# Optimization experiments

Hardware: AMD Instinct MI355X
Metric: run time of the kernel (lower is better)

## Reference

```python
import jax, jax.numpy as jnp
import numpy as np
from jax import lax

# config constants (match init_kwargs)
SEQ_LEN = 512
PRED_LEN = 96
ENC_IN = 64
D_MODEL = 128
E_LAYERS = 2
GRAPH_SCALE = 16
GRAPH_RANK = 8
TCN_KERNEL = 3
TCN_DILATION = 2
BATCH = 16


def setup_inputs() -> dict:
    key = jax.random.key(0)
    ks = jax.random.split(key, 12)
    s = 0.02
    inp = {
        "x_enc": jax.random.normal(ks[0], (BATCH, SEQ_LEN, ENC_IN), jnp.float32),
        "x_mark_enc": jnp.zeros((BATCH, SEQ_LEN, 4), jnp.float32),
        "x_dec": jnp.zeros((BATCH, PRED_LEN, ENC_IN), jnp.float32),
        "x_mark_dec": jnp.zeros((BATCH, PRED_LEN, 4), jnp.float32),
        # value embedding (scalar -> d_model)
        "w_emb": jax.random.normal(ks[1], (1, D_MODEL), jnp.float32) * s,
        "b_emb": jnp.zeros((D_MODEL,), jnp.float32),
        # stacked dilated causal conv layers [L, K, Cin, Cout]
        "conv_w": jax.random.normal(ks[2], (E_LAYERS, TCN_KERNEL, D_MODEL, D_MODEL), jnp.float32) * s,
        "conv_b": jnp.zeros((E_LAYERS, D_MODEL), jnp.float32),
        # low-rank graph generator projections
        "gg_w1": jax.random.normal(ks[3], (D_MODEL, GRAPH_RANK), jnp.float32) * s,
        "gg_b1": jnp.zeros((GRAPH_RANK,), jnp.float32),
        "gg_w2": jax.random.normal(ks[4], (D_MODEL, GRAPH_RANK), jnp.float32) * s,
        "gg_b2": jnp.zeros((GRAPH_RANK,), jnp.float32),
        # head: Linear(d_model * num_tokens, pred_len)
        "head_w": jax.random.normal(ks[5], (D_MODEL * SEQ_LEN, PRED_LEN), jnp.float32) * s,
        "head_b": jnp.zeros((PRED_LEN,), jnp.float32),
    }
    return inp


def _tcn(x_enc, w_emb, b_emb, conv_w, conv_b):
    # x_enc: [B, L, N] -> channel-independent per-variable encoding -> [B, N, L, D]
    B, L, N = x_enc.shape
    h = x_enc.transpose(0, 2, 1).reshape(B * N, L, 1) @ w_emb + b_emb  # [B*N, L, D]
    for i in range(conv_w.shape[0]):
        dil = TCN_DILATION ** i
        pad = (TCN_KERNEL - 1) * dil
        hp = jnp.pad(h, ((0, 0), (pad, 0), (0, 0)))  # causal left pad
        y = lax.conv_general_dilated(
            hp, conv_w[i], window_strides=(1,), padding="VALID",
            rhs_dilation=(dil,), dimension_numbers=("NWC", "WIO", "NWC"),
        ) + conv_b[i]
        h = jax.nn.gelu(y) + h  # residual
    return h.reshape(B, N, L, -1)


def _forward(x_enc, w_emb, b_emb, conv_w, conv_b, gg_w1, gg_b1, gg_w2, gg_b2, head_w, head_b):
    h_time = _tcn(x_enc, w_emb, b_emb, conv_w, conv_b)  # [B, N, L, D]
    B, N, L, D = h_time.shape
    S = L // GRAPH_SCALE  # number of segments (L divisible by scale)
    h_seg = h_time.reshape(B, N, S, GRAPH_SCALE, D)
    z = h_seg.mean(axis=3)  # [B, N, S, D] segment summaries
    # low-rank graph generation for all segments at once
    e1 = z @ gg_w1 + gg_b1  # [B, N, S, r]
    e2 = z @ gg_w2 + gg_b2
    scores = jnp.einsum("bnsr,bmsr->bsnm", e1, e2) / jnp.asarray(np.sqrt(GRAPH_RANK), z.dtype)
    adj = jax.nn.softmax(scores, axis=-1)  # [B, S, N, N] row-stochastic
    # adjacency temporal-smoothness regularizer: sum_s mean|adj_s - adj_{s-1}|
    reg = jnp.sum(jnp.mean(jnp.abs(adj[:, 1:] - adj[:, :-1]), axis=(0, 2, 3)))
    # graph-weighted feature mixing per segment
    h_mix = jnp.einsum("bsnm,bmscd->bnscd", adj, h_seg).reshape(B, N, L, D)
    # head over flattened (token, dim)
    out = h_mix.reshape(B, N, L * D) @ head_w + head_b  # [B, N, pred_len]
    return out.transpose(0, 2, 1), reg  # [B, pred_len, N]


def reference(x_enc, x_mark_enc, x_dec, x_mark_dec, w_emb, b_emb, conv_w, conv_b,
              gg_w1, gg_b1, gg_w2, gg_b2, head_w, head_b):
    # x_mark_enc / x_dec / x_mark_dec are unused by forecast path (faithful to source)
    return _forward(x_enc, w_emb, b_emb, conv_w, conv_b, gg_w1, gg_b1, gg_w2, gg_b2, head_w, head_b)
```

## Files before the change

### kernel.cpp

```cpp
#include <hip/hip_runtime.h>
#include <hip/hip_bf16.h>


#define BATCH 16
#define SEQ 512
#define NVAR 64
#define DM 128
#define SEG 32
#define SCL 16
#define RNK 8
#define PRED 96
#define BN (BATCH * NVAR)
#define ROWLEN (SEQ * DM)

typedef unsigned short ushort_t;
typedef __attribute__((ext_vector_type(8))) short short8;
typedef __attribute__((ext_vector_type(4))) float f32x4;

__device__ inline float bf2f(ushort_t u) {
    union { unsigned int i; float f; } x;
    x.i = ((unsigned int)u) << 16;
    return x.f;
}
__device__ inline ushort_t f2bf(float f) {
    union { float f; unsigned int i; } u;
    u.f = f;
    unsigned int x = u.i;
    return (ushort_t)((x + 0x7fffu + ((x >> 16) & 1u)) >> 16);
}
__device__ inline unsigned int pkbf(float a, float b) {
    __hip_bfloat162 h = __float22bfloat162_rn(make_float2(a, b));
    union { __hip_bfloat162 h2; unsigned int u; } c;
    c.h2 = h;
    return c.u;
}
__device__ inline float blo(unsigned int u) {
    union { unsigned int i; float f; } x;
    x.i = u << 16;
    return x.f;
}
__device__ inline float bhi(unsigned int u) {
    union { unsigned int i; float f; } x;
    x.i = u & 0xFFFF0000u;
    return x.f;
}
__device__ inline float gelu_fast(float x) {
    float x2 = x * x;
    float t2 = x * fmaf(-0.10294854f, x2, -2.3022584f);
    float e;
    asm("v_exp_f32 %0, %1" : "=v"(e) : "v"(t2));
    return x * __builtin_amdgcn_rcpf(1.0f + e);
}

__global__ __launch_bounds__(256) void prep(
    const float* __restrict__ conv_w, const float* __restrict__ w_emb,
    const float* __restrict__ b_emb, const float* __restrict__ conv_b,
    const float* __restrict__ head_w, const float* __restrict__ head_b,
    ushort_t* __restrict__ WTf, float* __restrict__ Acoef,
    float* __restrict__ Bias3, ushort_t* __restrict__ HWf,
    float* __restrict__ out, float* __restrict__ regacc) {
    __shared__ float ts[32 * 97];
    int bid = blockIdx.x;
    if (bid == 0 && threadIdx.x == 0) regacc[0] = 0.f;
    if (bid < 512) {
        int bx = bid >> 7, ci = bid & 127;
        if (threadIdx.x < 128) {
            int co = threadIdx.x;
            if (bx < 3) {
                int kt = ci >> 5, quad = (ci >> 3) & 3, j = ci & 7;
                int ng = co >> 4, col = co & 15;
                int lane = quad * 16 + col;
                WTf[((((size_t)bx * 4 + kt) * 8 + ng) * 64 + lane) * 8 + j] =
                    f2bf(conv_w[(size_t)(3 + bx) * 16384 + (size_t)ci * 128 + co]);
            } else if (ci == 0) {
                float a0 = 0.f, a1 = 0.f, a2 = 0.f, c0 = 0.f, c1 = 0.f, c2 = 0.f;
                for (int k = 0; k < 128; ++k) {
                    float we = w_emb[k], be = b_emb[k];
                    float w0 = conv_w[((size_t)(0 * 128 + k)) * 128 + co];
                    float w1 = conv_w[((size_t)(1 * 128 + k)) * 128 + co];
                    float w2 = conv_w[((size_t)(2 * 128 + k)) * 128 + co];
                    a0 += we * w0; c0 += be * w0;
                    a1 += we * w1; c1 += be * w1;
                    a2 += we * w2; c2 += be * w2;
                }
                Acoef[0 * 128 + co] = a0;
                Acoef[1 * 128 + co] = a1;
                Acoef[2 * 128 + co] = a2;
                float b0 = conv_b[co];
                Bias3[0 * 128 + co] = b0 + c2;
                Bias3[1 * 128 + co] = b0 + c1 + c2;
                Bias3[2 * 128 + co] = b0 + c0 + c1 + c2;
            }
        }
    } else if (bid < 1536) {
        int k32p = bid - 512;
        int s = k32p >> 5, t = k32p & 31;
        int kbase = (s * 64 + t) * 32;
        const float* src = head_w + (size_t)kbase * 96;
        for (int idx = threadIdx.x; idx < 3072; idx += 256) {
            int kk = idx / 96, p = idx - kk * 96;
            ts[kk * 97 + p] = src[idx];
        }
        __syncthreads();
        unsigned int* ob32 =
            reinterpret_cast<unsigned int*>(HWf + (size_t)k32p * 3072);
        for (int odx = threadIdx.x; odx < 1536; odx += 256) {
            int p = odx >> 4, kk = (odx & 15) * 2;
            ob32[odx] = pkbf(ts[kk * 97 + p], ts[(kk + 1) * 97 + p]);
        }
    } else {
        int idx = (bid - 1536) * 256 + threadIdx.x;
        if (idx < BATCH * PRED * NVAR) {
            int p = (idx >> 6) % PRED;
            out[idx] = head_b[p];
        }
    }
}

__global__ __launch_bounds__(256) void hw_prep(
    const float* __restrict__ head_w, ushort_t* __restrict__ HWf, int kh) {
    __shared__ float ts[32 * 97];
    int k32p = blockIdx.x;
    int s = k32p >> 5, t = k32p & 31;
    int kbase = (s * 64 + kh * 32 + t) * 32;
    const float* src = head_w + (size_t)kbase * 96;
    for (int idx = threadIdx.x; idx < 3072; idx += 256) {
        int kk = idx / 96, p = idx - kk * 96;
        ts[kk * 97 + p] = src[idx];
    }
    __syncthreads();
    unsigned int* ob32 =
        reinterpret_cast<unsigned int*>(HWf + (size_t)k32p * 3072);
    for (int odx = threadIdx.x; odx < 1536; odx += 256) {
        int p = odx >> 4, kk = (odx & 15) * 2;
        ob32[odx] = pkbf(ts[kk * 97 + p], ts[(kk + 1) * 97 + p]);
    }
}

__global__ __launch_bounds__(256, 4) void tcn_mfma(
    const float* __restrict__ x, const float* __restrict__ w_emb,
    const float* __restrict__ b_emb, const float* __restrict__ Acoef,
    const float* __restrict__ Bias3, const ushort_t* __restrict__ WTf,
    const float* __restrict__ conv_b,
    const float* __restrict__ gw1, const float* __restrict__ gb1,
    const float* __restrict__ gw2, const float* __restrict__ gb2,
    ushort_t* __restrict__ h2, float* __restrict__ e1, float* __restrict__ e2) {
    __shared__ __align__(16) ushort_t h1s[68 * 136];
    __shared__ float xs[70];
    __shared__ float zbuf[4 * 136];

    int bn = blockIdx.x;
    int b = bn >> 6, n = bn & 63;
    int chunk = blockIdx.y;
    int l0 = chunk * 64;
    int tid = threadIdx.x;

    {
        const float* xb = x + (size_t)b * SEQ * NVAR + n;
        if (tid < 70) {
            int l = l0 - 6 + tid;
            xs[tid] = (l >= 0) ? xb[(size_t)l * NVAR] : 0.0f;
        }
    }
    __syncthreads();

    {
        int dp = (tid & 63) * 2;
        float2 A0 = *reinterpret_cast<const float2*>(&Acoef[0 * 128 + dp]);
        float2 A1 = *reinterpret_cast<const float2*>(&Acoef[1 * 128 + dp]);
        float2 A2 = *reinterpret_cast<const float2*>(&Acoef[2 * 128 + dp]);
        float2 BF = *reinterpret_cast<const float2*>(&Bias3[2 * 128 + dp]);
        float2 we2 = *reinterpret_cast<const float2*>(&w_emb[dp]);
        float2 be2 = *reinterpret_cast<const float2*>(&b_emb[dp]);
#pragma unroll
        for (int i = 0; i < 17; ++i) {
            int row = (tid >> 6) + 4 * i;
            int l = l0 - 4 + row;
            unsigned int pk = 0;
            if (l >= 0) {
                float x0 = xs[row], x1 = xs[row + 1], x2 = xs[row + 2];
                float2 bias = BF;
                if (l < 2)
                    bias = *reinterpret_cast<const float2*>(&Bias3[l * 128 + dp]);
                float y0 = fmaf(x0, A0.x, fmaf(x1, A1.x, fmaf(x2, A2.x, bias.x)));
                float y1 = fmaf(x0, A0.y, fmaf(x1, A1.y, fmaf(x2, A2.y, bias.y)));
                float r0 = gelu_fast(y0) + fmaf(x2, we2.x, be2.x);
                float r1 = gelu_fast(y1) + fmaf(x2, we2.y, be2.y);
                pk = pkbf(r0, r1);
            }
            *reinterpret_cast<unsigned int*>(&h1s[row * 136 + dp]) = pk;
        }
    }
    __syncthreads();

    int lane = tid & 63;
    int wv = tid >> 6;
    int quad = lane >> 4;
    int col = lane & 15;
    int cobase = wv * 32;

    f32x4 acc2[4][2];
#pragma unroll
    for (int mt = 0; mt < 4; ++mt)
#pragma unroll
        for (int nt = 0; nt < 2; ++nt)
            acc2[mt][nt] = (f32x4){0.f, 0.f, 0.f, 0.f};

#pragma unroll
    for (int tap = 0; tap < 3; ++tap) {
        short8 wf0[4], wf1[4];
#pragma unroll
        for (int kt = 0; kt < 4; ++kt) {
            const ushort_t* bp =
                WTf + ((((size_t)tap * 4 + kt) * 8 + wv * 2) * 64 + lane) * 8;
            wf0[kt] = *(const short8*)bp;
            wf1[kt] = *(const short8*)(bp + 512);
        }
#pragma unroll
        for (int kt = 0; kt < 4; ++kt) {
            int kc = kt * 32 + quad * 8;
#pragma unroll
            for (int mt = 0; mt < 4; ++mt) {
                short8 hf = *(const short8*)&h1s[(mt * 16 + col + 2 * tap) * 136 + kc];
                acc2[mt][0] = __builtin_amdgcn_mfma_f32_16x16x32_bf16(wf0[kt], hf, acc2[mt][0], 0, 0, 0);
                acc2[mt][1] = __builtin_amdgcn_mfma_f32_16x16x32_bf16(wf1[kt], hf, acc2[mt][1], 0, 0, 0);
            }
        }
    }

    {
        uint2 res[4][2];
#pragma unroll
        for (int mt = 0; mt < 4; ++mt) {
            int li = mt * 16 + col;
#pragma unroll
            for (int nt = 0; nt < 2; ++nt) {
                int co = cobase + nt * 16 + quad * 4;
                res[mt][nt] = *reinterpret_cast<const uint2*>(
                    &h1s[(li + 4) * 136 + co]);
            }
        }
        __syncthreads();
        float4 bias[2];
        bias[0] = *reinterpret_cast<const float4*>(&conv_b[DM + cobase + quad * 4]);
        bias[1] = *reinterpret_cast<const float4*>(&conv_b[DM + cobase + 16 + quad * 4]);
#pragma unroll
        for (int mt = 0; mt < 4; ++mt) {
            int li = mt * 16 + col;
#pragma unroll
            for (int nt = 0; nt < 2; ++nt) {
                int co = cobase + nt * 16 + quad * 4;
                float h0 = gelu_fast(acc2[mt][nt][0] + bias[nt].x) + blo(res[mt][nt].x);
                float h1 = gelu_fast(acc2[mt][nt][1] + bias[nt].y) + bhi(res[mt][nt].x);
                float h2v = gelu_fast(acc2[mt][nt][2] + bias[nt].z) + blo(res[mt][nt].y);
                float h3 = gelu_fast(acc2[mt][nt][3] + bias[nt].w) + bhi(res[mt][nt].y);
                uint2 pk;
                pk.x = pkbf(h0, h1);
                pk.y = pkbf(h2v, h3);
                *reinterpret_cast<uint2*>(&h1s[li * 136 + co]) = pk;
            }
        }
    }
    __syncthreads();

    {
        ushort_t* orow = h2 + (size_t)bn * ROWLEN + (size_t)l0 * 128;
#pragma unroll
        for (int i = 0; i < 4; ++i) {
            int q = tid + 256 * i;
            int row = q >> 4, c8 = (q & 15) * 8;
            *(short8*)&orow[row * 128 + c8] = *(const short8*)&h1s[row * 136 + c8];
        }
    }
    {
        int sl = tid >> 6;
        int dp = (tid & 63) * 2;
        float a0 = 0.0f, a1 = 0.0f;
#pragma unroll
        for (int c = 0; c < SCL; ++c) {
            unsigned int u = *reinterpret_cast<const unsigned int*>(
                &h1s[(sl * 16 + c) * 136 + dp]);
            a0 += blo(u);
            a1 += bhi(u);
        }
        zbuf[sl * 136 + dp] = a0 * 0.0625f;
        zbuf[sl * 136 + dp + 1] = a1 * 0.0625f;
    }
    __syncthreads();
    {
        int outi = tid >> 2;
        int part = tid & 3;
        int sl = outi >> 4;
        int which = (outi >> 3) & 1;
        int r = outi & 7;
        const float* w = which ? gw2 : gw1;
        float a = 0.0f;
#pragma unroll 8
        for (int i = 0; i < 32; ++i) {
            int d = i * 4 + part;
            a += zbuf[sl * 136 + d] * w[d * RNK + r];
        }
        a += __shfl_xor(a, 1, 64);
        a += __shfl_xor(a, 2, 64);
        if (part == 0) {
            a += (which ? gb2 : gb1)[r];
            int s = chunk * 4 + sl;
            (which ? e2 : e1)[(((size_t)b * SEG + s) * NVAR + n) * RNK + r] = a;
        }
    }
}

__global__ __launch_bounds__(256) void g_gemm(
    const ushort_t* __restrict__ h2, const ushort_t* __restrict__ HWf,
    float* __restrict__ G, int kh, int first) {
    __shared__ __align__(16) ushort_t As[2][64 * 72];
    int s = blockIdx.x;
    int bnt = blockIdx.y;
    int bn0 = bnt * 64;
    int kbase = kh * 1024;
    int lane = threadIdx.x & 63, wv = threadIdx.x >> 6;
    int quad = lane >> 4, col = lane & 15;
    int mh = wv & 1;
    int ph = wv >> 1;
    int p0 = ph * 48 + col;

    int arow = threadIdx.x >> 2, akq = (threadIdx.x & 3) * 16;
    const ushort_t* aptr =
        h2 + (size_t)(bn0 + arow) * ROWLEN + (size_t)s * 2048 + kbase + akq;
    const ushort_t* hb =
        HWf + (size_t)s * 98304 + (size_t)p0 * 32 + quad * 8;

    f32x4 acc[3][2];
#pragma unroll
    for (int i = 0; i < 3; ++i)
#pragma unroll
        for (int j = 0; j < 2; ++j) acc[i][j] = (f32x4){0.f, 0.f, 0.f, 0.f};

    short8 pa0 = *(const short8*)aptr;
    short8 pa1 = *(const short8*)(aptr + 8);
    short8 pf[2][2][3];
#pragma unroll
    for (int kk = 0; kk < 2; ++kk)
#pragma unroll
        for (int i = 0; i < 3; ++i)
            pf[0][kk][i] = *(const short8*)(hb + kk * 3072 + i * 512);
    *(short8*)&As[0][arow * 72 + akq] = pa0;
    *(short8*)&As[0][arow * 72 + akq + 8] = pa1;
    __syncthreads();

#pragma unroll
    for (int kt = 0; kt < 16; ++kt) {
        const int par = kt & 1;
        if (kt < 15) {
            const ushort_t* ap = aptr + (kt + 1) * 64;
            pa0 = *(const short8*)ap;
            pa1 = *(const short8*)(ap + 8);
            const ushort_t* fb = hb + (size_t)(kt + 1) * 6144;
#pragma unroll
            for (int kk = 0; kk < 2; ++kk)
#pragma unroll
                for (int i = 0; i < 3; ++i)
                    pf[par ^ 1][kk][i] =
                        *(const short8*)(fb + kk * 3072 + i * 512);
        }
#pragma unroll
        for (int kk = 0; kk < 2; ++kk) {
            int kc = kk * 32 + quad * 8;
#pragma unroll
            for (int j = 0; j < 2; ++j) {
                short8 bnfr =
                    *(const short8*)&As[par][(mh * 32 + j * 16 + col) * 72 + kc];
#pragma unroll
                for (int i = 0; i < 3; ++i)
                    acc[i][j] = __builtin_amdgcn_mfma_f32_16x16x32_bf16(
                        pf[par][kk][i], bnfr, acc[i][j], 0, 0, 0);
            }
        }
        if (kt < 15) {
            *(short8*)&As[par ^ 1][arow * 72 + akq] = pa0;
            *(short8*)&As[par ^ 1][arow * 72 + akq + 8] = pa1;
        }
        __syncthreads();
    }

#pragma unroll
    for (int i = 0; i < 3; ++i)
#pragma unroll
        for (int j = 0; j < 2; ++j)
#pragma unroll
            for (int r = 0; r < 4; ++r) {
                int p = ph * 48 + i * 16 + quad * 4 + r;
                int m = mh * 32 + j * 16 + col;
                size_t o = (((size_t)s * BATCH + bnt) * PRED + p) * NVAR + m;
                if (first) G[o] = acc[i][j][r];
                else G[o] += acc[i][j][r];
            }
}

__global__ __launch_bounds__(256) void out_mix(
    const float* __restrict__ e1, const float* __restrict__ e2,
    const float* __restrict__ G, float* __restrict__ out,
    float* __restrict__ regacc) {
    __shared__ float adjn[2][32][65];
    __shared__ float Gs[96][65];
    __shared__ float e2s[3][64][8];
    __shared__ float e1s[3][32][8];
    __shared__ float wsum[4];
    int b = blockIdx.x, sg = blockIdx.y, nh = blockIdx.z;
    int s0 = sg * 2;
    int wv = threadIdx.x >> 6, lane = threadIdx.x & 63;

    for (int idx = threadIdx.x; idx < 3 * 64 * 8; idx += 256) {
        int j = idx >> 9, m = (idx >> 3) & 63, r = idx & 7;
        int s = s0 - 1 + j;
        e2s[j][m][r] = (s >= 0)
            ? e2[(((size_t)b * SEG + s) * NVAR + m) * RNK + r] : 0.0f;
    }
    for (int idx = threadIdx.x; idx < 3 * 32 * 8; idx += 256) {
        int j = idx >> 8, nl = (idx >> 3) & 31, r = idx & 7;
        int s = s0 - 1 + j;
        e1s[j][nl][r] = (s >= 0)
            ? e1[(((size_t)b * SEG + s) * NVAR + nh * 32 + nl) * RNK + r] : 0.0f;
    }
    __syncthreads();

    float regsum = 0.0f;
    for (int t = 0; t < 8; ++t) {
        int nl = wv * 8 + t;
        float a[3];
#pragma unroll
        for (int j = 0; j < 3; ++j) {
            float sc = 0.0f;
#pragma unroll
            for (int r = 0; r < 8; ++r) sc += e1s[j][nl][r] * e2s[j][lane][r];
            sc *= 0.35355339059327373f;
            float mx = sc;
            for (int off = 32; off; off >>= 1)
                mx = fmaxf(mx, __shfl_xor(mx, off, 64));
            float ex = __expf(sc - mx);
            float sm = ex;
            for (int off = 32; off; off >>= 1) sm += __shfl_xor(sm, off, 64);
            a[j] = ex * __builtin_amdgcn_rcpf(sm);
        }
        if (s0 > 0) regsum += fabsf(a[1] - a[0]);
        regsum += fabsf(a[2] - a[1]);
        adjn[0][nl][lane] = a[1];
        adjn[1][nl][lane] = a[2];
    }
    __syncthreads();

    int pg = threadIdx.x >> 4;
    int ng = threadIdx.x & 15;
    float acc[6][2];
#pragma unroll
    for (int j = 0; j < 6; ++j) { acc[j][0] = 0.f; acc[j][1] = 0.f; }

#pragma unroll
    for (int ss = 0; ss < 2; ++ss) {
        int s = s0 + ss;
#pragma unroll
        for (int i = 0; i < 6; ++i) {
            int q = threadIdx.x + 256 * i;
            int row = q >> 4, mq = (q & 15) * 4;
            float4 v = *reinterpret_cast<const float4*>(
                &G[(((size_t)s * BATCH + b) * PRED + row) * NVAR + mq]);
            Gs[row][mq + 0] = v.x; Gs[row][mq + 1] = v.y;
            Gs[row][mq + 2] = v.z; Gs[row][mq + 3] = v.w;
        }
        __syncthreads();
#pragma unroll 4
        for (int m = 0; m < 64; ++m) {
            float a0 = adjn[ss][ng * 2 + 0][m];
            float a1 = adjn[ss][ng * 2 + 1][m];
#pragma unroll
            for (int j = 0; j < 6; ++j) {
                float g = Gs[pg * 6 + j][m];
                acc[j][0] += g * a0;
                acc[j][1] += g * a1;
            }
        }
        __syncthreads();
    }
#pragma unroll
    for (int j = 0; j < 6; ++j)
#pragma unroll
        for (int i = 0; i < 2; ++i) {
            int p = pg * 6 + j, n = nh * 32 + ng * 2 + i;
            atomicAdd(&out[((size_t)b * PRED + p) * NVAR + n], acc[j][i]);
        }
    for (int off = 32; off; off >>= 1) regsum += __shfl_xor(regsum, off, 64);
    if (lane == 0) wsum[wv] = regsum;
    __syncthreads();
    if (threadIdx.x == 0)
        atomicAdd(regacc, wsum[0] + wsum[1] + wsum[2] + wsum[3]);
}

__global__ void fin(const float* __restrict__ regacc, float* __restrict__ out,
                    int out_size) {
    out[out_size - 1] = regacc[0] * (1.0f / 65536.0f);
}

extern "C" void kernel_launch(void* const* d_in, const int* in_sizes, int n_in,
                              void* d_out, int out_size, void* d_ws,
                              size_t ws_size, hipStream_t stream) {
    const float* x_enc  = (const float*)d_in[0];
    const float* w_emb  = (const float*)d_in[4];
    const float* b_emb  = (const float*)d_in[5];
    const float* conv_w = (const float*)d_in[6];
    const float* conv_b = (const float*)d_in[7];
    const float* gg_w1  = (const float*)d_in[8];
    const float* gg_b1  = (const float*)d_in[9];
    const float* gg_w2  = (const float*)d_in[10];
    const float* gg_b2  = (const float*)d_in[11];
    const float* head_w = (const float*)d_in[12];
    const float* head_b = (const float*)d_in[13];
    float* out = (float*)d_out;

    char* ws = (char*)d_ws;
    ushort_t* h2   = (ushort_t*)(ws);
    float* G       = (float*)(ws + 134217728);
    float* e1      = (float*)(ws + 146800640);
    float* e2      = (float*)(ws + 147849216);
    ushort_t* WTf  = (ushort_t*)(ws + 148897792);
    float* Acoef   = (float*)(ws + 148996096);
    float* Bias3   = (float*)(ws + 148997632);
    ushort_t* HWf  = (ushort_t*)(ws + 149000192);
    float* regacc  = (float*)(ws + 157286400);

    prep<<<1920, 256, 0, stream>>>(
        conv_w, w_emb, b_emb, conv_b, head_w, head_b,
        WTf, Acoef, Bias3, HWf, out, regacc);
    tcn_mfma<<<dim3(BN, SEQ / 64), 256, 0, stream>>>(
        x_enc, w_emb, b_emb, Acoef, Bias3, WTf, conv_b,
        gg_w1, gg_b1, gg_w2, gg_b2, h2, e1, e2);
    g_gemm<<<dim3(SEG, BATCH), 256, 0, stream>>>(h2, HWf, G, 0, 1);
    hw_prep<<<1024, 256, 0, stream>>>(head_w, HWf, 1);
    g_gemm<<<dim3(SEG, BATCH), 256, 0, stream>>>(h2, HWf, G, 1, 0);
    out_mix<<<dim3(BATCH, 16, 2), 256, 0, stream>>>(
        e1, e2, G, out, regacc);
    fin<<<1, 1, 0, stream>>>(regacc, out, out_size);
}
```

Before: 292.5 us.

## Fuse head GEMM with graph mixing and convert full head weight upfront

Merges the two half-K head GEMM passes, the separate head-weight conversion for the second half, and the out_mix kernel into one g_out kernel per (batch, segment). The full-K product now stays in shared memory instead of going through a global G buffer. The softmax adjacency and regulariser are computed alongside it, and prep converts all of head_w in one launch. This removes G round trips and several launches, at the cost of fewer blocks (512) each doing a longer K loop, and more atomics into out.

```diff
diff --git a/kernel.cpp b/kernel.cpp
--- a/kernel.cpp
+++ b/kernel.cpp
@@ -92,11 +92,9 @@
                 Bias3[2 * 128 + co] = b0 + c0 + c1 + c2;
             }
         }
-    } else if (bid < 1536) {
+    } else if (bid < 2560) {
         int k32p = bid - 512;
-        int s = k32p >> 5, t = k32p & 31;
-        int kbase = (s * 64 + t) * 32;
-        const float* src = head_w + (size_t)kbase * 96;
+        const float* src = head_w + (size_t)k32p * 32 * 96;
         for (int idx = threadIdx.x; idx < 3072; idx += 256) {
             int kk = idx / 96, p = idx - kk * 96;
             ts[kk * 97 + p] = src[idx];
@@ -109,31 +107,11 @@
             ob32[odx] = pkbf(ts[kk * 97 + p], ts[(kk + 1) * 97 + p]);
         }
     } else {
-        int idx = (bid - 1536) * 256 + threadIdx.x;
+        int idx = (bid - 2560) * 256 + threadIdx.x;
         if (idx < BATCH * PRED * NVAR) {
             int p = (idx >> 6) % PRED;
             out[idx] = head_b[p];
         }
-    }
-}
-
-__global__ __launch_bounds__(256) void hw_prep(
-    const float* __restrict__ head_w, ushort_t* __restrict__ HWf, int kh) {
-    __shared__ float ts[32 * 97];
-    int k32p = blockIdx.x;
-    int s = k32p >> 5, t = k32p & 31;
-    int kbase = (s * 64 + kh * 32 + t) * 32;
-    const float* src = head_w + (size_t)kbase * 96;
-    for (int idx = threadIdx.x; idx < 3072; idx += 256) {
-        int kk = idx / 96, p = idx - kk * 96;
-        ts[kk * 97 + p] = src[idx];
-    }
-    __syncthreads();
-    unsigned int* ob32 =
-        reinterpret_cast<unsigned int*>(HWf + (size_t)k32p * 3072);
-    for (int odx = threadIdx.x; odx < 1536; odx += 256) {
-        int p = odx >> 4, kk = (odx & 15) * 2;
-        ob32[odx] = pkbf(ts[kk * 97 + p], ts[(kk + 1) * 97 + p]);
     }
 }
 
@@ -310,25 +288,43 @@
     }
 }
 
-__global__ __launch_bounds__(256) void g_gemm(
+__global__ __launch_bounds__(256) void g_out(
     const ushort_t* __restrict__ h2, const ushort_t* __restrict__ HWf,
-    float* __restrict__ G, int kh, int first) {
+    const float* __restrict__ e1, const float* __restrict__ e2,
+    float* __restrict__ out, float* __restrict__ regacc) {
     __shared__ __align__(16) ushort_t As[2][64 * 72];
-    int s = blockIdx.x;
-    int bnt = blockIdx.y;
-    int bn0 = bnt * 64;
-    int kbase = kh * 1024;
-    int lane = threadIdx.x & 63, wv = threadIdx.x >> 6;
+    __shared__ __align__(16) float Gs[96][66];
+    __shared__ float e1s[2][64][9];
+    __shared__ float e2s[2][64][9];
+    __shared__ float wsum[4];
+    float* adjn = reinterpret_cast<float*>(As);
+
+    int b = blockIdx.x, s = blockIdx.y;
+    int tid = threadIdx.x;
+    int lane = tid & 63, wv = tid >> 6;
     int quad = lane >> 4, col = lane & 15;
     int mh = wv & 1;
     int ph = wv >> 1;
     int p0 = ph * 48 + col;
 
-    int arow = threadIdx.x >> 2, akq = (threadIdx.x & 3) * 16;
+    for (int idx = tid; idx < 1024; idx += 256) {
+        int j = idx >> 9, mm = (idx >> 3) & 63, r = idx & 7;
+        int ss = s - 1 + j;
+        float v1 = 0.f, v2 = 0.f;
+        if (ss >= 0) {
+            size_t o = (((size_t)b * SEG + ss) * NVAR + mm) * RNK + r;
+            v1 = e1[o];
+            v2 = e2[o];
+        }
+        e1s[j][mm][r] = v1;
+        e2s[j][mm][r] = v2;
+    }
+
+    int arow = tid >> 2, akq = (tid & 3) * 16;
     const ushort_t* aptr =
-        h2 + (size_t)(bn0 + arow) * ROWLEN + (size_t)s * 2048 + kbase + akq;
+        h2 + (size_t)(b * 64 + arow) * ROWLEN + (size_t)s * 2048 + akq;
     const ushort_t* hb =
-        HWf + (size_t)s * 98304 + (size_t)p0 * 32 + quad * 8;
+        HWf + (size_t)s * 196608 + (size_t)p0 * 32 + quad * 8;
 
     f32x4 acc[3][2];
 #pragma unroll
@@ -349,9 +345,9 @@
     __syncthreads();
 
 #pragma unroll
-    for (int kt = 0; kt < 16; ++kt) {
+    for (int kt = 0; kt < 32; ++kt) {
         const int par = kt & 1;
-        if (kt < 15) {
+        if (kt < 31) {
             const ushort_t* ap = aptr + (kt + 1) * 64;
             pa0 = *(const short8*)ap;
             pa1 = *(const short8*)(ap + 8);
@@ -376,7 +372,7 @@
                         pf[par][kk][i], bnfr, acc[i][j], 0, 0, 0);
             }
         }
-        if (kt < 15) {
+        if (kt < 31) {
             *(short8*)&As[par ^ 1][arow * 72 + akq] = pa0;
             *(short8*)&As[par ^ 1][arow * 72 + akq + 8] = pa1;
         }
@@ -388,110 +384,73 @@
 #pragma unroll
         for (int j = 0; j < 2; ++j)
 #pragma unroll
-            for (int r = 0; r < 4; ++r) {
-                int p = ph * 48 + i * 16 + quad * 4 + r;
-                int m = mh * 32 + j * 16 + col;
-                size_t o = (((size_t)s * BATCH + bnt) * PRED + p) * NVAR + m;
-                if (first) G[o] = acc[i][j][r];
-                else G[o] += acc[i][j][r];
-            }
-}
-
-__global__ __launch_bounds__(256) void out_mix(
-    const float* __restrict__ e1, const float* __restrict__ e2,
-    const float* __restrict__ G, float* __restrict__ out,
-    float* __restrict__ regacc) {
-    __shared__ float adjn[2][32][65];
-    __shared__ float Gs[96][65];
-    __shared__ float e2s[3][64][8];
-    __shared__ float e1s[3][32][8];
-    __shared__ float wsum[4];
-    int b = blockIdx.x, sg = blockIdx.y, nh = blockIdx.z;
-    int s0 = sg * 2;
-    int wv = threadIdx.x >> 6, lane = threadIdx.x & 63;
-
-    for (int idx = threadIdx.x; idx < 3 * 64 * 8; idx += 256) {
-        int j = idx >> 9, m = (idx >> 3) & 63, r = idx & 7;
-        int s = s0 - 1 + j;
-        e2s[j][m][r] = (s >= 0)
-            ? e2[(((size_t)b * SEG + s) * NVAR + m) * RNK + r] : 0.0f;
-    }
-    for (int idx = threadIdx.x; idx < 3 * 32 * 8; idx += 256) {
-        int j = idx >> 8, nl = (idx >> 3) & 31, r = idx & 7;
-        int s = s0 - 1 + j;
-        e1s[j][nl][r] = (s >= 0)
-            ? e1[(((size_t)b * SEG + s) * NVAR + nh * 32 + nl) * RNK + r] : 0.0f;
-    }
-    __syncthreads();
+            for (int r = 0; r < 4; ++r)
+                Gs[ph * 48 + i * 16 + quad * 4 + r][mh * 32 + j * 16 + col] =
+                    acc[i][j][r];
 
     float regsum = 0.0f;
-    for (int t = 0; t < 8; ++t) {
-        int nl = wv * 8 + t;
-        float a[3];
-#pragma unroll
-        for (int j = 0; j < 3; ++j) {
-            float sc = 0.0f;
-#pragma unroll
-            for (int r = 0; r < 8; ++r) sc += e1s[j][nl][r] * e2s[j][lane][r];
-            sc *= 0.35355339059327373f;
-            float mx = sc;
-            for (int off = 32; off; off >>= 1)
-                mx = fmaxf(mx, __shfl_xor(mx, off, 64));
-            float ex = __expf(sc - mx);
-            float sm = ex;
-            for (int off = 32; off; off >>= 1) sm += __shfl_xor(sm, off, 64);
-            a[j] = ex * __builtin_amdgcn_rcpf(sm);
-        }
-        if (s0 > 0) regsum += fabsf(a[1] - a[0]);
-        regsum += fabsf(a[2] - a[1]);
-        adjn[0][nl][lane] = a[1];
-        adjn[1][nl][lane] = a[2];
-    }
-    __syncthreads();
-
-    int pg = threadIdx.x >> 4;
-    int ng = threadIdx.x & 15;
-    float acc[6][2];
-#pragma unroll
-    for (int j = 0; j < 6; ++j) { acc[j][0] = 0.f; acc[j][1] = 0.f; }
-
-#pragma unroll
-    for (int ss = 0; ss < 2; ++ss) {
-        int s = s0 + ss;
-#pragma unroll
-        for (int i = 0; i < 6; ++i) {
-            int q = threadIdx.x + 256 * i;
-            int row = q >> 4, mq = (q & 15) * 4;
-            float4 v = *reinterpret_cast<const float4*>(
-                &G[(((size_t)s * BATCH + b) * PRED + row) * NVAR + mq]);
-            Gs[row][mq + 0] = v.x; Gs[row][mq + 1] = v.y;
-            Gs[row][mq + 2] = v.z; Gs[row][mq + 3] = v.w;
-        }
-        __syncthreads();
+    for (int t = 0; t < 16; ++t) {
+        int nl = wv * 16 + t;
+        float scC = 0.0f, scP = 0.0f;
+#pragma unroll
+        for (int r = 0; r < 8; ++r) {
+            scC += e1s[1][nl][r] * e2s[1][lane][r];
+            scP += e1s[0][nl][r] * e2s[0][lane][r];
+        }
+        scC *= 0.35355339059327373f;
+        scP *= 0.35355339059327373f;
+        float mxC = scC, mxP = scP;
+        for (int off = 32; off; off >>= 1) {
+            mxC = fmaxf(mxC, __shfl_xor(mxC, off, 64));
+            mxP = fmaxf(mxP, __shfl_xor(mxP, off, 64));
+        }
+        float exC = __expf(scC - mxC), exP = __expf(scP - mxP);
+        float smC = exC, smP = exP;
+        for (int off = 32; off; off >>= 1) {
+            smC += __shfl_xor(smC, off, 64);
+            smP += __shfl_xor(smP, off, 64);
+        }
+        float aC = exC * __builtin_amdgcn_rcpf(smC);
+        if (s > 0) regsum += fabsf(aC - exP * __builtin_amdgcn_rcpf(smP));
+        adjn[nl * 66 + lane] = aC;
+    }
+    __syncthreads();
+
+    {
+        int pg = tid >> 4;
+        int ng = tid & 15;
+        float ao[6][4];
+#pragma unroll
+        for (int j = 0; j < 6; ++j)
+#pragma unroll
+            for (int i = 0; i < 4; ++i) ao[j][i] = 0.f;
 #pragma unroll 4
-        for (int m = 0; m < 64; ++m) {
-            float a0 = adjn[ss][ng * 2 + 0][m];
-            float a1 = adjn[ss][ng * 2 + 1][m];
+        for (int m = 0; m < 64; m += 2) {
+            float2 av[4];
+#pragma unroll
+            for (int i = 0; i < 4; ++i)
+                av[i] = *reinterpret_cast<const float2*>(
+                    &adjn[(ng * 4 + i) * 66 + m]);
 #pragma unroll
             for (int j = 0; j < 6; ++j) {
-                float g = Gs[pg * 6 + j][m];
-                acc[j][0] += g * a0;
-                acc[j][1] += g * a1;
-            }
-        }
-        __syncthreads();
-    }
-#pragma unroll
-    for (int j = 0; j < 6; ++j)
-#pragma unroll
-        for (int i = 0; i < 2; ++i) {
-            int p = pg * 6 + j, n = nh * 32 + ng * 2 + i;
-            atomicAdd(&out[((size_t)b * PRED + p) * NVAR + n], acc[j][i]);
-        }
+                float2 g = *reinterpret_cast<const float2*>(&Gs[pg * 6 + j][m]);
+#pragma unroll
+                for (int i = 0; i < 4; ++i)
+                    ao[j][i] = fmaf(g.x, av[i].x, fmaf(g.y, av[i].y, ao[j][i]));
+            }
+        }
+#pragma unroll
+        for (int j = 0; j < 6; ++j)
+#pragma unroll
+            for (int i = 0; i < 4; ++i)
+                atomicAdd(&out[((size_t)b * PRED + pg * 6 + j) * NVAR +
+                               ng * 4 + i],
+                          ao[j][i]);
+    }
     for (int off = 32; off; off >>= 1) regsum += __shfl_xor(regsum, off, 64);
     if (lane == 0) wsum[wv] = regsum;
     __syncthreads();
-    if (threadIdx.x == 0)
+    if (tid == 0)
         atomicAdd(regacc, wsum[0] + wsum[1] + wsum[2] + wsum[3]);
 }
 
@@ -518,25 +477,21 @@
 
     char* ws = (char*)d_ws;
     ushort_t* h2   = (ushort_t*)(ws);
-    float* G       = (float*)(ws + 134217728);
-    float* e1      = (float*)(ws + 146800640);
-    float* e2      = (float*)(ws + 147849216);
-    ushort_t* WTf  = (ushort_t*)(ws + 148897792);
-    float* Acoef   = (float*)(ws + 148996096);
-    float* Bias3   = (float*)(ws + 148997632);
-    ushort_t* HWf  = (ushort_t*)(ws + 149000192);
+    float* e1      = (float*)(ws + 134217728);
+    float* e2      = (float*)(ws + 135266304);
+    ushort_t* WTf  = (ushort_t*)(ws + 136314880);
+    float* Acoef   = (float*)(ws + 136413184);
+    float* Bias3   = (float*)(ws + 136414720);
+    ushort_t* HWf  = (ushort_t*)(ws + 136416256);
     float* regacc  = (float*)(ws + 157286400);
 
-    prep<<<1920, 256, 0, stream>>>(
+    prep<<<2944, 256, 0, stream>>>(
         conv_w, w_emb, b_emb, conv_b, head_w, head_b,
         WTf, Acoef, Bias3, HWf, out, regacc);
     tcn_mfma<<<dim3(BN, SEQ / 64), 256, 0, stream>>>(
         x_enc, w_emb, b_emb, Acoef, Bias3, WTf, conv_b,
         gg_w1, gg_b1, gg_w2, gg_b2, h2, e1, e2);
-    g_gemm<<<dim3(SEG, BATCH), 256, 0, stream>>>(h2, HWf, G, 0, 1);
-    hw_prep<<<1024, 256, 0, stream>>>(head_w, HWf, 1);
-    g_gemm<<<dim3(SEG, BATCH), 256, 0, stream>>>(h2, HWf, G, 1, 0);
-    out_mix<<<dim3(BATCH, 16, 2), 256, 0, stream>>>(
-        e1, e2, G, out, regacc);
+    g_out<<<dim3(BATCH, SEG), 256, 0, stream>>>(
+        h2, HWf, e1, e2, out, regacc);
     fin<<<1, 1, 0, stream>>>(regacc, out, out_size);
 }
```

Result: slower. 307.9 us (+5.3%).
